# Kernel optimization log

Measured on AMD Instinct MI355X. Metric: run time of the kernel, lower is better.

## Reference

```python
import jax, jax.numpy as jnp
import numpy as np
from jax import lax

N, D, BATCH = 8192, 256, 64


def setup_inputs() -> dict:
    key = jax.random.key(0)
    V = jax.random.normal(key, (N, D), dtype=jnp.float32)
    V = V / jnp.linalg.norm(V, axis=1, keepdims=True)  # cosine = raw dot product
    return {
        "V": V,
        "cos_threshold": jnp.array([0.25], dtype=jnp.float32),
        "batch_size": BATCH,
    }


def reference(V, cos_threshold, batch_size):
    """Faithful port of Embeddings._fast_predict: batched cosine-sim thresholding
    followed by a sequential transitive merge of group ids.

    Returns group_ids [N] int32 (the clustering result; the torch code wraps this
    into a Matcher object, which is pure python bookkeeping).
    """
    n, d = V.shape
    B = int(batch_size)
    n_batches = n // B
    thr = cos_threshold[0]
    j_idx = jnp.arange(n, dtype=jnp.int32)
    group_init = jnp.arange(n, dtype=jnp.int32)

    def outer(gids, batch_start):
        # group ids as of the start of this batch (torch computes batch_matched
        # with these, but reads live group_ids inside the row loop via views)
        g0 = gids
        Vb = lax.dynamic_slice(V, (batch_start, 0), (B, d))        # [B, D]
        sims = Vb @ V.T                                            # [B, N]
        g0_i = lax.dynamic_slice(g0, (batch_start,), (B,))         # [B]
        jmask = j_idx > batch_start                                # j_slice = batch_start+1 .. N
        mask = (sims >= thr) & jmask[None, :] & (g0_i[:, None] != g0[None, :])  # [B, N]

        def inner(g, inp):
            k, row = inp
            gi = g[batch_start + k]  # live group id of row i (torch g_i is a view)
            # isin(group_ids, matched_groups): flag[label]=1 if any matched j has
            # current group label == label, then gather back through g
            flag = jnp.zeros(n, jnp.int32).at[g].max(row.astype(jnp.int32))
            g = jnp.where(flag[g] > 0, gi, g)
            return g, None

        gids, _ = lax.scan(inner, gids, (jnp.arange(B, dtype=jnp.int32), mask))
        return gids, None

    starts = jnp.arange(n_batches, dtype=jnp.int32) * B
    gids, _ = lax.scan(outer, group_init, starts)
    return gids
```

## Files before the change

### kernel.cpp

```cpp
#include <hip/hip_runtime.h>
#include <stdint.h>

#define NPTS 8192
#define DIM  256
#define CAP  32768
#define LDSE 8192
#define IBCAP 256
#define BAND 2.0e-3f

typedef _Float16 f16x8  __attribute__((ext_vector_type(8)));
typedef float    f32x16 __attribute__((ext_vector_type(16)));


__global__ __launch_bounds__(256) void convert_kernel(
        const float* __restrict__ V, _Float16* __restrict__ Vh,
        unsigned* __restrict__ ctr) {
    if (blockIdx.x == 0 && threadIdx.x == 0) { ctr[0] = 0u; ctr[1] = 0u; }
    size_t t = (size_t)blockIdx.x * 256 + threadIdx.x;
    const float4* src = reinterpret_cast<const float4*>(V) + t * 2;
    float4 v0 = src[0], v1 = src[1];
    f16x8 h;
    h[0] = (_Float16)v0.x; h[1] = (_Float16)v0.y;
    h[2] = (_Float16)v0.z; h[3] = (_Float16)v0.w;
    h[4] = (_Float16)v1.x; h[5] = (_Float16)v1.y;
    h[6] = (_Float16)v1.z; h[7] = (_Float16)v1.w;
    *reinterpret_cast<f16x8*>(Vh + t * 8) = h;
}

__global__ void init_count(unsigned* ctr) {
    if (threadIdx.x == 0) { ctr[0] = 0u; ctr[1] = 0u; }
}

__device__ __forceinline__ void gload_lds16(const void* g, void* l) {
    __builtin_amdgcn_global_load_lds(
        (const __attribute__((address_space(1))) void*)g,
        (__attribute__((address_space(3))) void*)l, 16, 0, 0);
}

__global__ __launch_bounds__(256, 4) void edge_mfma(
        const _Float16* __restrict__ Vh,
        const float* __restrict__ V,
        const float* __restrict__ thr_p,
        unsigned* __restrict__ ctr,
        unsigned* __restrict__ edges) {
    int t = blockIdx.x;
    int bi = (int)(64.5f - sqrtf(64.5f * 64.5f - 2.0f * (float)t));
    while (bi * 64 - (bi * (bi - 1)) / 2 > t) --bi;
    while ((bi + 1) * 64 - ((bi + 1) * bi) / 2 <= t) ++bi;
    int bj = bi + (t - (bi * 64 - (bi * (bi - 1)) / 2));

    __shared__ _Float16 L[2 * 128 * 64];
    __shared__ unsigned ibl[IBCAP];
    __shared__ unsigned ibn;

    const float thr = thr_p[0];
    const float hi = thr + BAND, lo = thr - BAND;
    const int tid  = threadIdx.x;
    const int lane = tid & 63;
    const int wid  = tid >> 6;
    const int wr = wid >> 1, wc = wid & 1;
    const int i0 = bi * 128, j0 = bj * 128;

    if (tid == 0) ibn = 0u;

    f32x16 acc[2][2];
#pragma unroll
    for (int a = 0; a < 2; ++a)
#pragma unroll
        for (int b = 0; b < 2; ++b) acc[a][b] = 0.0f;

    const int row_l = lane >> 3;
    const int bphys = lane & 7;
    const int l31 = lane & 31, g = lane >> 5, l7 = lane & 7;

    for (int kc = 0; kc < DIM; kc += 64) {
#pragma unroll
        for (int q = 0; q < 8; ++q) {
            const int qq  = wid * 8 + q;
            const int arr = qq >> 4;
            const int ins = qq & 15;
            const int row = ins * 8 + row_l;
            const int blk = bphys ^ row_l;
            const int grow = (arr ? j0 : i0) + row;
            gload_lds16(Vh + ((size_t)grow * DIM + kc + blk * 8),
                        &L[arr * 8192 + ins * 512]);
        }
        __syncthreads();

#pragma unroll
        for (int s = 0; s < 4; ++s) {
            const int xa = (((s * 2 + g) ^ l7) << 3);
            f16x8 ah[2], bh[2];
#pragma unroll
            for (int a = 0; a < 2; ++a) {
                ah[a] = *(const f16x8*)&L[(wr * 64 + a * 32 + l31) * 64 + xa];
                bh[a] = *(const f16x8*)&L[8192 + (wc * 64 + a * 32 + l31) * 64 + xa];
            }
#pragma unroll
            for (int a = 0; a < 2; ++a)
#pragma unroll
                for (int b = 0; b < 2; ++b)
                    acc[a][b] = __builtin_amdgcn_mfma_f32_32x32x16_f16(
                        ah[a], bh[b], acc[a][b], 0, 0, 0);
        }
        __syncthreads();
    }

    const int rbase = 4 * (lane >> 5);
#pragma unroll
    for (int a = 0; a < 2; ++a)
#pragma unroll
        for (int b = 0; b < 2; ++b)
#pragma unroll
            for (int reg = 0; reg < 16; ++reg) {
                float sim = acc[a][b][reg];
                int row = (reg & 3) + 8 * (reg >> 2) + rbase;
                int i = i0 + wr * 64 + a * 32 + row;
                int j = j0 + wc * 64 + b * 32 + l31;
                if (j > i && sim >= lo) {
                    unsigned key = ((unsigned)i << 13) | (unsigned)j;
                    if (sim >= hi) {
                        unsigned p = atomicAdd(&ctr[0], 1u);
                        if (p < CAP) edges[p] = key;
                    } else {
                        unsigned p = atomicAdd(&ibn, 1u);
                        if (p < IBCAP) ibl[p] = key;
                    }
                }
            }
    __syncthreads();

    unsigned nib = ibn; if (nib > IBCAP) nib = IBCAP;
    const double thrd = (double)thr;
    for (unsigned q = tid; q < nib; q += 256) {
        unsigned key = ibl[q];
        int i = (int)(key >> 13), j = (int)(key & 8191u);
        const float4* a4 = reinterpret_cast<const float4*>(V + (size_t)i * DIM);
        const float4* b4 = reinterpret_cast<const float4*>(V + (size_t)j * DIM);
        double s = 0.0;
#pragma unroll 4
        for (int k = 0; k < DIM / 4; ++k) {
            float4 x = a4[k], y = b4[k];
            s += (double)x.x * y.x + (double)x.y * y.y
               + (double)x.z * y.z + (double)x.w * y.w;
        }
        if (s >= thrd) {
            unsigned p = atomicAdd(&ctr[0], 1u);
            if (p < CAP) edges[p] = key;
        }
    }
}

__global__ __launch_bounds__(256) void edge_kernel(
        const float* __restrict__ V,
        const float* __restrict__ thr_p,
        unsigned*    __restrict__ ctr,
        unsigned*    __restrict__ edges) {
    const int bi = blockIdx.y, bj = blockIdx.x;
    if (bj < bi) return;

    __shared__ float As[128 * 32];
    __shared__ float Bs[128 * 32];

    const float thr = thr_p[0];
    const int tid = threadIdx.x;
    const int tx = tid & 15, ty = tid >> 4;
    const int i0 = bi * 128, j0 = bj * 128;

    float acc[8][8];
#pragma unroll
    for (int r = 0; r < 8; ++r)
#pragma unroll
        for (int c = 0; c < 8; ++c) acc[r][c] = 0.f;

    const int srow = tid >> 3, sq = tid & 7;

    for (int kc = 0; kc < DIM; kc += 32) {
#pragma unroll
        for (int p = 0; p < 4; ++p) {
            int row = srow + 32 * p;
            float4 va = *reinterpret_cast<const float4*>(
                &V[(size_t)(i0 + row) * DIM + kc + sq * 4]);
            float4 vb = *reinterpret_cast<const float4*>(
                &V[(size_t)(j0 + row) * DIM + kc + sq * 4]);
            int w = row * 32 + ((sq ^ ((row >> 3) & 7)) << 2);
            *reinterpret_cast<float4*>(&As[w]) = va;
            *reinterpret_cast<float4*>(&Bs[w]) = vb;
        }
        __syncthreads();
#pragma unroll
        for (int k4 = 0; k4 < 8; ++k4) {
            const float* pA = &As[(ty * 8) * 32 + ((k4 ^ (ty & 7)) << 2)];
            const float* pB = &Bs[(tx * 8) * 32 + ((k4 ^ (tx & 7)) << 2)];
            float4 a[8], b[8];
#pragma unroll
            for (int r = 0; r < 8; ++r)
                a[r] = *reinterpret_cast<const float4*>(&pA[r * 32]);
#pragma unroll
            for (int c = 0; c < 8; ++c)
                b[c] = *reinterpret_cast<const float4*>(&pB[c * 32]);
#pragma unroll
            for (int r = 0; r < 8; ++r)
#pragma unroll
                for (int c = 0; c < 8; ++c) {
                    acc[r][c] = fmaf(a[r].x, b[c].x, acc[r][c]);
                    acc[r][c] = fmaf(a[r].y, b[c].y, acc[r][c]);
                    acc[r][c] = fmaf(a[r].z, b[c].z, acc[r][c]);
                    acc[r][c] = fmaf(a[r].w, b[c].w, acc[r][c]);
                }
        }
        __syncthreads();
    }
#pragma unroll
    for (int r = 0; r < 8; ++r)
#pragma unroll
        for (int c = 0; c < 8; ++c) {
            int i = i0 + ty * 8 + r;
            int j = j0 + tx * 8 + c;
            if (j > i && acc[r][c] >= thr) {
                unsigned p = atomicAdd(&ctr[0], 1u);
                if (p < CAP) edges[p] = ((unsigned)i << 13) | (unsigned)j;
            }
        }
}

__global__ __launch_bounds__(1024) void uf_kernel(
        const unsigned* __restrict__ ctr,
        const unsigned* __restrict__ edges,
        int* __restrict__ out) {
    __shared__ int      par[NPTS];
    __shared__ unsigned slotA[NPTS];
    __shared__ unsigned slotB[NPTS];
    __shared__ unsigned sedge[LDSE];

    const int tid = threadIdx.x;

    unsigned EC = ctr[0]; if (EC > LDSE) EC = LDSE;

    for (int t = tid; t < NPTS; t += 1024) {
        par[t] = t; slotA[t] = 0xFFFFFFFFu; slotB[t] = 0xFFFFFFFFu;
    }
    for (unsigned e = tid; e < EC; e += 1024) sedge[e] = edges[e];
    __syncthreads();

    volatile int* vpar = par;

    for (int round = 0;; ++round) {
        unsigned* S = (round & 1) ? slotB : slotA;
        unsigned* T = (round & 1) ? slotA : slotB;

        for (unsigned e = tid; e < EC; e += 1024) {
            unsigned key = sedge[e];
            if (key & 0x80000000u) continue;
            int ri = (int)(key >> 13), rj = (int)(key & 8191u);
            int p;
            while ((p = vpar[ri]) != ri) ri = p;
            while ((p = vpar[rj]) != rj) rj = p;
            atomicMin(&S[ri], key);
            atomicMin(&S[rj], key);
        }
        __syncthreads();

        int mylive = 0;
        for (unsigned e = tid; e < EC; e += 1024) {
            unsigned key = sedge[e];
            if (key & 0x80000000u) continue;
            int i = (int)(key >> 13), j = (int)(key & 8191u);
            int ri = i, rj = j, p;
            while ((p = vpar[ri]) != ri) ri = p;
            while ((p = vpar[rj]) != rj) rj = p;
            if (S[ri] == key && S[rj] == key) {
                if (ri != rj) { par[rj] = ri; par[i] = ri; par[j] = ri; }
                sedge[e] = key | 0x80000000u;
            } else {
                mylive = 1;
            }
        }
        for (int t = tid; t < NPTS; t += 1024) T[t] = 0xFFFFFFFFu;
        if (__syncthreads_count(mylive) == 0) break;
    }

    for (int t = tid; t < NPTS; t += 1024) {
        int r = t, p;
        while ((p = par[r]) != r) r = p;
        out[t] = r;
    }
}

extern "C" void kernel_launch(void* const* d_in, const int* in_sizes, int n_in,
                              void* d_out, int out_size, void* d_ws, size_t ws_size,
                              hipStream_t stream) {
    const float* V     = (const float*)d_in[0];
    const float* thr_p = (const float*)d_in[1];

    unsigned* ctr   = (unsigned*)d_ws;
    unsigned* edges = (unsigned*)((char*)d_ws + 64);
    int*      out   = (int*)d_out;

    const size_t vhOff = 1u << 20;
    const size_t vN    = (size_t)NPTS * DIM;
    const size_t need  = vhOff + vN * sizeof(_Float16) + 65536;

    if (ws_size >= need) {
        _Float16* Vh = (_Float16*)((char*)d_ws + vhOff);
        hipLaunchKernelGGL(convert_kernel, dim3(1024), dim3(256), 0, stream,
                           V, Vh, ctr);
        hipLaunchKernelGGL(edge_mfma, dim3(2080), dim3(256), 0, stream,
                           Vh, V, thr_p, ctr, edges);
    } else {
        hipLaunchKernelGGL(init_count, dim3(1), dim3(64), 0, stream, ctr);
        hipLaunchKernelGGL(edge_kernel, dim3(64, 64), dim3(256), 0, stream,
                           V, thr_p, ctr, edges);
    }
    hipLaunchKernelGGL(uf_kernel, dim3(1), dim3(1024), 0, stream,
                       ctr, edges, out);
}
```

Before: 99.68 us.

## Enlarge edge MFMA tile to 256x256 with double-buffered LDS staging

The similarity tile per block grows from 128x128 to 256x256, handled by 8 waves (512 threads), each computing a 128x64 sub-tile. This cuts the block count from 2080 to 528 and reduces redundant global loads. The K loop is unrolled with two LDS buffers so the next chunk loads while the current one computes. The cost is 128KB of LDS per block and more accumulator registers, which lowers occupancy, and fewer blocks may leave CUs underused. Blocks on the diagonal also waste more work.

```diff
diff --git a/kernel.cpp b/kernel.cpp
--- a/kernel.cpp
+++ b/kernel.cpp
@@ -37,19 +37,19 @@
         (__attribute__((address_space(3))) void*)l, 16, 0, 0);
 }
 
-__global__ __launch_bounds__(256, 4) void edge_mfma(
+__global__ __launch_bounds__(512, 2) void edge_mfma(
         const _Float16* __restrict__ Vh,
         const float* __restrict__ V,
         const float* __restrict__ thr_p,
         unsigned* __restrict__ ctr,
         unsigned* __restrict__ edges) {
     int t = blockIdx.x;
-    int bi = (int)(64.5f - sqrtf(64.5f * 64.5f - 2.0f * (float)t));
-    while (bi * 64 - (bi * (bi - 1)) / 2 > t) --bi;
-    while ((bi + 1) * 64 - ((bi + 1) * bi) / 2 <= t) ++bi;
-    int bj = bi + (t - (bi * 64 - (bi * (bi - 1)) / 2));
-
-    __shared__ _Float16 L[2 * 128 * 64];
+    int bi = (int)(32.5f - sqrtf(32.5f * 32.5f - 2.0f * (float)t));
+    while (bi * 32 - (bi * (bi - 1)) / 2 > t) --bi;
+    while ((bi + 1) * 32 - ((bi + 1) * bi) / 2 <= t) ++bi;
+    int bj = bi + (t - (bi * 32 - (bi * (bi - 1)) / 2));
+
+    __shared__ _Float16 L[2][32768];
     __shared__ unsigned ibl[IBCAP];
     __shared__ unsigned ibn;
 
@@ -58,64 +58,71 @@
     const int tid  = threadIdx.x;
     const int lane = tid & 63;
     const int wid  = tid >> 6;
-    const int wr = wid >> 1, wc = wid & 1;
-    const int i0 = bi * 128, j0 = bj * 128;
+    const int wr = wid >> 2, wc = wid & 3;
+    const int i0 = bi * 256, j0 = bj * 256;
 
     if (tid == 0) ibn = 0u;
 
-    f32x16 acc[2][2];
-#pragma unroll
-    for (int a = 0; a < 2; ++a)
+    f32x16 acc[4][2];
+#pragma unroll
+    for (int a = 0; a < 4; ++a)
 #pragma unroll
         for (int b = 0; b < 2; ++b) acc[a][b] = 0.0f;
 
     const int row_l = lane >> 3;
     const int bphys = lane & 7;
     const int l31 = lane & 31, g = lane >> 5, l7 = lane & 7;
-
-    for (int kc = 0; kc < DIM; kc += 64) {
+    const int cblk = bphys ^ row_l;
+
+    auto STAGE = [&](int buf, int kc) {
 #pragma unroll
         for (int q = 0; q < 8; ++q) {
             const int qq  = wid * 8 + q;
-            const int arr = qq >> 4;
-            const int ins = qq & 15;
-            const int row = ins * 8 + row_l;
-            const int blk = bphys ^ row_l;
-            const int grow = (arr ? j0 : i0) + row;
-            gload_lds16(Vh + ((size_t)grow * DIM + kc + blk * 8),
-                        &L[arr * 8192 + ins * 512]);
-        }
-        __syncthreads();
-
+            const int arr = qq >> 5;
+            const int ins = qq & 31;
+            const int grow = (arr ? j0 : i0) + ins * 8 + row_l;
+            gload_lds16(Vh + ((size_t)grow * DIM + kc + cblk * 8),
+                        &L[buf][arr * 16384 + ins * 512]);
+        }
+    };
+
+    auto COMPUTE = [&](int buf) {
 #pragma unroll
         for (int s = 0; s < 4; ++s) {
             const int xa = (((s * 2 + g) ^ l7) << 3);
-            f16x8 ah[2], bh[2];
-#pragma unroll
-            for (int a = 0; a < 2; ++a) {
-                ah[a] = *(const f16x8*)&L[(wr * 64 + a * 32 + l31) * 64 + xa];
-                bh[a] = *(const f16x8*)&L[8192 + (wc * 64 + a * 32 + l31) * 64 + xa];
-            }
-#pragma unroll
-            for (int a = 0; a < 2; ++a)
+            f16x8 af[4], bf[2];
+#pragma unroll
+            for (int a = 0; a < 4; ++a)
+                af[a] = *(const f16x8*)&L[buf][(wr * 128 + a * 32 + l31) * 64 + xa];
+#pragma unroll
+            for (int b = 0; b < 2; ++b)
+                bf[b] = *(const f16x8*)&L[buf][16384 + (wc * 64 + b * 32 + l31) * 64 + xa];
+#pragma unroll
+            for (int a = 0; a < 4; ++a)
 #pragma unroll
                 for (int b = 0; b < 2; ++b)
                     acc[a][b] = __builtin_amdgcn_mfma_f32_32x32x16_f16(
-                        ah[a], bh[b], acc[a][b], 0, 0, 0);
-        }
-        __syncthreads();
-    }
-
-    const int rbase = 4 * (lane >> 5);
-#pragma unroll
-    for (int a = 0; a < 2; ++a)
+                        af[a], bf[b], acc[a][b], 0, 0, 0);
+        }
+    };
+
+    STAGE(0, 0);
+    __syncthreads();
+    STAGE(1, 64);  COMPUTE(0); __syncthreads();
+    STAGE(0, 128); COMPUTE(1); __syncthreads();
+    STAGE(1, 192); COMPUTE(0); __syncthreads();
+    COMPUTE(1);
+    __syncthreads();
+
+#pragma unroll
+    for (int a = 0; a < 4; ++a)
 #pragma unroll
         for (int b = 0; b < 2; ++b)
 #pragma unroll
             for (int reg = 0; reg < 16; ++reg) {
                 float sim = acc[a][b][reg];
-                int row = (reg & 3) + 8 * (reg >> 2) + rbase;
-                int i = i0 + wr * 64 + a * 32 + row;
+                int rr = (reg & 3) + 8 * (reg >> 2) + 4 * g;
+                int i = i0 + wr * 128 + a * 32 + rr;
                 int j = j0 + wc * 64 + b * 32 + l31;
                 if (j > i && sim >= lo) {
                     unsigned key = ((unsigned)i << 13) | (unsigned)j;
@@ -132,7 +139,7 @@
 
     unsigned nib = ibn; if (nib > IBCAP) nib = IBCAP;
     const double thrd = (double)thr;
-    for (unsigned q = tid; q < nib; q += 256) {
+    for (unsigned q = tid; q < nib; q += 512) {
         unsigned key = ibl[q];
         int i = (int)(key >> 13), j = (int)(key & 8191u);
         const float4* a4 = reinterpret_cast<const float4*>(V + (size_t)i * DIM);
@@ -305,7 +312,7 @@
         _Float16* Vh = (_Float16*)((char*)d_ws + vhOff);
         hipLaunchKernelGGL(convert_kernel, dim3(1024), dim3(256), 0, stream,
                            V, Vh, ctr);
-        hipLaunchKernelGGL(edge_mfma, dim3(2080), dim3(256), 0, stream,
+        hipLaunchKernelGGL(edge_mfma, dim3(528), dim3(512), 0, stream,
                            Vh, V, thr_p, ctr, edges);
     } else {
         hipLaunchKernelGGL(init_count, dim3(1), dim3(64), 0, stream, ctr);
```

Measured after the change: 108.7 us. 1.09x slower.

## Pre-tile fp16 V into MFMA fragment layout and load operands directly from global

Applied to the files above, without the earlier changes.

The convert kernel now writes V in fp16 using a tiled layout, so each lane's MFMA operand fragment is one contiguous 16-byte chunk. The edge kernel no longer stages tiles through LDS with barriers. It loads A/B fragments straight from global memory into registers, prefetching the next k-step while the current MFMAs run. This removes LDS traffic and the __syncthreads calls, but each wave now reads its operands from global/L2 on its own, with no sharing through LDS.

```diff
diff --git a/kernel.cpp b/kernel.cpp
--- a/kernel.cpp
+++ b/kernel.cpp
@@ -13,10 +13,11 @@
 
 
 __global__ __launch_bounds__(256) void convert_kernel(
-        const float* __restrict__ V, _Float16* __restrict__ Vh,
+        const float* __restrict__ V, _Float16* __restrict__ Vt,
         unsigned* __restrict__ ctr) {
     if (blockIdx.x == 0 && threadIdx.x == 0) { ctr[0] = 0u; ctr[1] = 0u; }
     size_t t = (size_t)blockIdx.x * 256 + threadIdx.x;
+    int row = (int)(t >> 5), q = (int)(t & 31);
     const float4* src = reinterpret_cast<const float4*>(V) + t * 2;
     float4 v0 = src[0], v1 = src[1];
     f16x8 h;
@@ -24,21 +25,17 @@
     h[2] = (_Float16)v0.z; h[3] = (_Float16)v0.w;
     h[4] = (_Float16)v1.x; h[5] = (_Float16)v1.y;
     h[6] = (_Float16)v1.z; h[7] = (_Float16)v1.w;
-    *reinterpret_cast<f16x8*>(Vh + t * 8) = h;
+    size_t dst = ((size_t)(row >> 5) * 16 + (unsigned)(q >> 1)) * 512
+               + (size_t)(row & 31) * 16 + (size_t)(q & 1) * 8;
+    *reinterpret_cast<f16x8*>(Vt + dst) = h;
 }
 
 __global__ void init_count(unsigned* ctr) {
     if (threadIdx.x == 0) { ctr[0] = 0u; ctr[1] = 0u; }
 }
 
-__device__ __forceinline__ void gload_lds16(const void* g, void* l) {
-    __builtin_amdgcn_global_load_lds(
-        (const __attribute__((address_space(1))) void*)g,
-        (__attribute__((address_space(3))) void*)l, 16, 0, 0);
-}
-
 __global__ __launch_bounds__(256, 4) void edge_mfma(
-        const _Float16* __restrict__ Vh,
+        const _Float16* __restrict__ Vt,
         const float* __restrict__ V,
         const float* __restrict__ thr_p,
         unsigned* __restrict__ ctr,
@@ -49,7 +46,6 @@
     while ((bi + 1) * 64 - ((bi + 1) * bi) / 2 <= t) ++bi;
     int bj = bi + (t - (bi * 64 - (bi * (bi - 1)) / 2));
 
-    __shared__ _Float16 L[2 * 128 * 64];
     __shared__ unsigned ibl[IBCAP];
     __shared__ unsigned ibn;
 
@@ -62,6 +58,13 @@
     const int i0 = bi * 128, j0 = bj * 128;
 
     if (tid == 0) ibn = 0u;
+    __syncthreads();
+
+    const int l31 = lane & 31, g = lane >> 5;
+    const int co = ((l31 << 1) | g) << 3;
+
+    const _Float16* pA = Vt + (size_t)((i0 >> 5) + wr * 2) * 8192 + co;
+    const _Float16* pB = Vt + (size_t)((j0 >> 5) + wc * 2) * 8192 + co;
 
     f32x16 acc[2][2];
 #pragma unroll
@@ -69,44 +72,27 @@
 #pragma unroll
         for (int b = 0; b < 2; ++b) acc[a][b] = 0.0f;
 
-    const int row_l = lane >> 3;
-    const int bphys = lane & 7;
-    const int l31 = lane & 31, g = lane >> 5, l7 = lane & 7;
-
-    for (int kc = 0; kc < DIM; kc += 64) {
-#pragma unroll
-        for (int q = 0; q < 8; ++q) {
-            const int qq  = wid * 8 + q;
-            const int arr = qq >> 4;
-            const int ins = qq & 15;
-            const int row = ins * 8 + row_l;
-            const int blk = bphys ^ row_l;
-            const int grow = (arr ? j0 : i0) + row;
-            gload_lds16(Vh + ((size_t)grow * DIM + kc + blk * 8),
-                        &L[arr * 8192 + ins * 512]);
-        }
-        __syncthreads();
-
-#pragma unroll
-        for (int s = 0; s < 4; ++s) {
-            const int xa = (((s * 2 + g) ^ l7) << 3);
-            f16x8 ah[2], bh[2];
-#pragma unroll
-            for (int a = 0; a < 2; ++a) {
-                ah[a] = *(const f16x8*)&L[(wr * 64 + a * 32 + l31) * 64 + xa];
-                bh[a] = *(const f16x8*)&L[8192 + (wc * 64 + a * 32 + l31) * 64 + xa];
-            }
-#pragma unroll
-            for (int a = 0; a < 2; ++a)
-#pragma unroll
-                for (int b = 0; b < 2; ++b)
-                    acc[a][b] = __builtin_amdgcn_mfma_f32_32x32x16_f16(
-                        ah[a], bh[b], acc[a][b], 0, 0, 0);
-        }
-        __syncthreads();
-    }
-
-    const int rbase = 4 * (lane >> 5);
+    f16x8 a0 = *(const f16x8*)(pA);
+    f16x8 a1 = *(const f16x8*)(pA + 8192);
+    f16x8 b0 = *(const f16x8*)(pB);
+    f16x8 b1 = *(const f16x8*)(pB + 8192);
+#pragma unroll
+    for (int s = 0; s < 16; ++s) {
+        f16x8 na0, na1, nb0, nb1;
+        if (s < 15) {
+            const int o = (s + 1) * 512;
+            na0 = *(const f16x8*)(pA + o);
+            na1 = *(const f16x8*)(pA + 8192 + o);
+            nb0 = *(const f16x8*)(pB + o);
+            nb1 = *(const f16x8*)(pB + 8192 + o);
+        }
+        acc[0][0] = __builtin_amdgcn_mfma_f32_32x32x16_f16(a0, b0, acc[0][0], 0, 0, 0);
+        acc[0][1] = __builtin_amdgcn_mfma_f32_32x32x16_f16(a0, b1, acc[0][1], 0, 0, 0);
+        acc[1][0] = __builtin_amdgcn_mfma_f32_32x32x16_f16(a1, b0, acc[1][0], 0, 0, 0);
+        acc[1][1] = __builtin_amdgcn_mfma_f32_32x32x16_f16(a1, b1, acc[1][1], 0, 0, 0);
+        if (s < 15) { a0 = na0; a1 = na1; b0 = nb0; b1 = nb1; }
+    }
+
 #pragma unroll
     for (int a = 0; a < 2; ++a)
 #pragma unroll
@@ -114,8 +100,8 @@
 #pragma unroll
             for (int reg = 0; reg < 16; ++reg) {
                 float sim = acc[a][b][reg];
-                int row = (reg & 3) + 8 * (reg >> 2) + rbase;
-                int i = i0 + wr * 64 + a * 32 + row;
+                int rr = (reg & 3) + 8 * (reg >> 2) + 4 * g;
+                int i = i0 + wr * 64 + a * 32 + rr;
                 int j = j0 + wc * 64 + b * 32 + l31;
                 if (j > i && sim >= lo) {
                     unsigned key = ((unsigned)i << 13) | (unsigned)j;
@@ -297,16 +283,16 @@
     unsigned* edges = (unsigned*)((char*)d_ws + 64);
     int*      out   = (int*)d_out;
 
-    const size_t vhOff = 1u << 20;
+    const size_t vtOff = 1u << 20;
     const size_t vN    = (size_t)NPTS * DIM;
-    const size_t need  = vhOff + vN * sizeof(_Float16) + 65536;
+    const size_t need  = vtOff + vN * sizeof(_Float16) + 65536;
 
     if (ws_size >= need) {
-        _Float16* Vh = (_Float16*)((char*)d_ws + vhOff);
+        _Float16* Vt = (_Float16*)((char*)d_ws + vtOff);
         hipLaunchKernelGGL(convert_kernel, dim3(1024), dim3(256), 0, stream,
-                           V, Vh, ctr);
+                           V, Vt, ctr);
         hipLaunchKernelGGL(edge_mfma, dim3(2080), dim3(256), 0, stream,
-                           Vh, V, thr_p, ctr, edges);
+                           Vt, V, thr_p, ctr, edges);
     } else {
         hipLaunchKernelGGL(init_count, dim3(1), dim3(64), 0, stream, ctr);
         hipLaunchKernelGGL(edge_kernel, dim3(64, 64), dim3(256), 0, stream,
```

Measured after the change: 100.4 us. No clear change (+0.7%).
